# Optimization experiments

Measured on AMD Instinct MI355X. Metric: run time of the kernel, lower is better.

## Reference

```python
import jax, jax.numpy as jnp
import numpy as np

N_NODES = 100000
N_EDGES = 1600000
IN_CH = 64
HID = 64
OUT_CH = 128
EDGE_CH = 3
OBS_RANGE = 0.5
ATK_RANGE = 0.3


def setup_inputs() -> dict:
    key = jax.random.key(0)
    k = jax.random.split(key, 8)
    # node features: first column is an integer node type in {0,1,2}
    node_type = jax.random.randint(k[0], (N_NODES, 1), 0, 3).astype(jnp.float32)
    feats = jax.random.normal(k[1], (N_NODES, IN_CH - 1), dtype=jnp.float32)
    x = jnp.concatenate([node_type, feats], axis=-1)
    edge_index = jax.random.randint(k[2], (2, N_EDGES), 0, N_NODES)
    # edge_attr[:,0] = distance in [0,1)
    edge_attr = jax.random.uniform(k[3], (N_EDGES, EDGE_CH), dtype=jnp.float32)
    s1 = 1.0 / np.sqrt(2 * IN_CH + EDGE_CH)
    s2 = 1.0 / np.sqrt(HID)
    W1 = jax.random.normal(k[4], (2 * IN_CH + EDGE_CH, HID), dtype=jnp.float32) * s1
    b1 = jnp.zeros((HID,), dtype=jnp.float32)
    W2 = jax.random.normal(k[5], (HID, OUT_CH), dtype=jnp.float32) * s2
    b2 = jnp.zeros((OUT_CH,), dtype=jnp.float32)
    return {"x": x, "edge_index": edge_index, "edge_attr": edge_attr,
            "W1": W1, "b1": b1, "W2": W2, "b2": b2}


def reference(x, edge_index, edge_attr, W1, b1, W2, b2):
    src = edge_index[0]  # j (source)
    dst = edge_index[1]  # i (target)
    x_j = x[src]         # [E, IN_CH]
    x_i = x[dst]         # [E, IN_CH]
    h = jnp.concatenate([x_i, x_j, edge_attr], axis=-1)  # [E, 2*IN_CH+3]
    msg = jax.nn.relu(h @ W1 + b1) @ W2 + b2             # [E, OUT_CH]
    dist = edge_attr[:, 0]
    ntype = x_j[:, 0]
    mask = jnp.where(ntype == 0, dist < OBS_RANGE,
                     jnp.where(ntype == 1, dist < ATK_RANGE, True))
    msg = mask[:, None].astype(msg.dtype) * msg
    out = jax.ops.segment_sum(msg, dst, num_segments=x.shape[0])  # [N, OUT_CH]
    return jax.nn.relu(out)
```

## Files before the change

kernel.cpp:

```cpp
#include <hip/hip_runtime.h>

#define N_NODES 100000
#define N_EDGES 1600000
#define IN_CH   64
#define HID_CH  64
#define OUT_CH  128
#define TILE    128
#define N_TILES (N_EDGES / TILE)

typedef __attribute__((ext_vector_type(8))) __bf16    bf16x8;
typedef __attribute__((ext_vector_type(4))) float     f32x4;
typedef __attribute__((ext_vector_type(2))) _Float16  f16x2;
typedef __attribute__((ext_vector_type(8))) _Float16  f16x8;

__device__ __forceinline__ unsigned short f2bf(float f) {
    union { float f; unsigned int i; } c;
    c.f = f;
    unsigned int u = c.i;
    unsigned int r = (u + 0x7FFFu + ((u >> 16) & 1u)) >> 16;
    return (unsigned short)r;
}

__device__ __forceinline__ void atomic_pk_add_f16(unsigned int* addr, f16x2 val) {
    typedef __attribute__((address_space(1))) f16x2 gf16x2;
    __builtin_amdgcn_global_atomic_fadd_v2f16((gf16x2*)(void*)addr, val);
}

__global__ void gnn_prep(const float* __restrict__ xf,
                         unsigned short* __restrict__ xb,
                         uint4* __restrict__ hz,
                         float4* __restrict__ cz) {
    int i = blockIdx.x * blockDim.x + threadIdx.x;
    if (i < 1600000) {
        float4 v = reinterpret_cast<const float4*>(xf)[i];
        ushort4 o;
        o.x = f2bf(v.x); o.y = f2bf(v.y); o.z = f2bf(v.z); o.w = f2bf(v.w);
        reinterpret_cast<ushort4*>(xb)[i] = o;
    } else if (i < 2400000) {
        hz[i - 1600000] = (uint4){0u, 0u, 0u, 0u};
    } else if (i < 2425000) {
        cz[i - 2400000] = (float4){0.f, 0.f, 0.f, 0.f};
    }
}

__global__ __launch_bounds__(256, 4) void gnn_edge_hidden(
    const float*          __restrict__ x,
    const unsigned short* __restrict__ xb,
    const int*            __restrict__ eidx,
    const float*          __restrict__ ea,
    const float*          __restrict__ W1,
    const float*          __restrict__ b1,
    unsigned int*         __restrict__ hsum,
    float*                __restrict__ cnt)
{
    __shared__ __align__(16) unsigned short W1T[64][136];
    __shared__ float w1tail[4][64];
    __shared__ float eas[128][4];
    __shared__ float masks[128];
    __shared__ int   dsts[128];
    __shared__ int   srcs[128];

    const int tid  = threadIdx.x;
    const int wave = tid >> 6;
    const int lane = tid & 63;
    const int q    = lane >> 4;
    const int m16  = lane & 15;

    for (int idx = tid; idx < 128 * 64; idx += 256) {
        int k = idx >> 6, n = idx & 63;
        W1T[n][k] = f2bf(W1[idx]);
    }
    if (tid < 64) {
        w1tail[0][tid] = W1[128 * 64 + tid];
        w1tail[1][tid] = W1[129 * 64 + tid];
        w1tail[2][tid] = W1[130 * 64 + tid];
        w1tail[3][tid] = b1[tid];
    }

    for (int t = blockIdx.x; t < N_TILES; t += gridDim.x) {
        __syncthreads();
        if (tid < 128) {
            int e = t * TILE + tid;
            int s = eidx[e];
            int d = eidx[N_EDGES + e];
            srcs[tid] = s;
            dsts[tid] = d;
            float a0 = ea[e * 3 + 0];
            float a1 = ea[e * 3 + 1];
            float a2 = ea[e * 3 + 2];
            eas[tid][0] = a0; eas[tid][1] = a1; eas[tid][2] = a2;
            float nt = x[(size_t)s * IN_CH];
            float mk;
            if (nt == 0.0f)      mk = (a0 < 0.5f) ? 1.0f : 0.0f;
            else if (nt == 1.0f) mk = (a0 < 0.3f) ? 1.0f : 0.0f;
            else                 mk = 1.0f;
            masks[tid] = mk;
            if (mk != 0.0f) unsafeAtomicAdd(&cnt[d], 1.0f);
        }
        __syncthreads();

        const int ebase = wave * 32;

        f32x4 acc1[2][4];
#pragma unroll
        for (int mt = 0; mt < 2; ++mt) {
            float e0[4], e1[4], e2[4];
#pragma unroll
            for (int r = 0; r < 4; ++r) {
                int el = ebase + mt * 16 + q * 4 + r;
                e0[r] = eas[el][0]; e1[r] = eas[el][1]; e2[r] = eas[el][2];
            }
#pragma unroll
            for (int nt = 0; nt < 4; ++nt) {
                int n = nt * 16 + m16;
                float t0 = w1tail[0][n], t1 = w1tail[1][n];
                float t2 = w1tail[2][n], bb = w1tail[3][n];
#pragma unroll
                for (int r = 0; r < 4; ++r)
                    acc1[mt][nt][r] = bb + e0[r] * t0 + e1[r] * t1 + e2[r] * t2;
            }
        }

#pragma unroll
        for (int kc = 0; kc < 4; ++kc) {
            bf16x8 af[2];
#pragma unroll
            for (int mt = 0; mt < 2; ++mt) {
                int el   = ebase + mt * 16 + m16;
                int node = (kc < 2) ? dsts[el] : srcs[el];
                af[mt] = *reinterpret_cast<const bf16x8*>(
                    xb + (size_t)node * IN_CH + (kc & 1) * 32 + q * 8);
            }
#pragma unroll
            for (int nt = 0; nt < 4; ++nt) {
                bf16x8 bfr = *reinterpret_cast<const bf16x8*>(
                    &W1T[nt * 16 + m16][kc * 32 + q * 8]);
                acc1[0][nt] = __builtin_amdgcn_mfma_f32_16x16x32_bf16(af[0], bfr, acc1[0][nt], 0, 0, 0);
                acc1[1][nt] = __builtin_amdgcn_mfma_f32_16x16x32_bf16(af[1], bfr, acc1[1][nt], 0, 0, 0);
            }
        }

#pragma unroll
        for (int mt = 0; mt < 2; ++mt) {
#pragma unroll
            for (int r = 0; r < 4; ++r) {
                int el = ebase + mt * 16 + q * 4 + r;
                float mk = masks[el];
                if (mk != 0.0f) {
                    unsigned int* hbase = hsum + (size_t)dsts[el] * 32;
                    float v0 = acc1[mt][0][r]; v0 = v0 > 0.f ? v0 : 0.f;
                    float v1 = acc1[mt][1][r]; v1 = v1 > 0.f ? v1 : 0.f;
                    float v2 = acc1[mt][2][r]; v2 = v2 > 0.f ? v2 : 0.f;
                    float v3 = acc1[mt][3][r]; v3 = v3 > 0.f ? v3 : 0.f;
                    if (v0 + v1 > 0.f) {
                        f16x2 p01 = {(_Float16)v0, (_Float16)v1};
                        atomic_pk_add_f16(hbase + m16, p01);
                    }
                    if (v2 + v3 > 0.f) {
                        f16x2 p23 = {(_Float16)v2, (_Float16)v3};
                        atomic_pk_add_f16(hbase + 16 + m16, p23);
                    }
                }
            }
        }
    }
}

__global__ __launch_bounds__(256, 4) void gnn_node_out(
    const _Float16* __restrict__ hsum,
    const float*    __restrict__ cnt,
    const float*    __restrict__ W2,
    const float*    __restrict__ b2,
    float*          __restrict__ out)
{
    __shared__ __align__(16) unsigned short W2T[128][72];
    __shared__ float b2s[128];

    const int tid  = threadIdx.x;
    const int wave = tid >> 6;
    const int lane = tid & 63;
    const int q    = lane >> 4;
    const int m16  = lane & 15;

    for (int idx = tid; idx < 64 * 128; idx += 256) {
        int p = idx >> 7, n = idx & 127;
        int ch = (p >> 1) + 16 * (p & 1) + ((p >= 32) ? 16 : 0);
        W2T[n][p] = f2bf(W2[ch * 128 + n]);
    }
    if (tid < 128) b2s[tid] = b2[tid];
    __syncthreads();

    const int nodeBase = (blockIdx.x * 4 + wave) * 32;
    if (nodeBase >= N_NODES) return;

    f32x4 acc[2][8];
#pragma unroll
    for (int mt = 0; mt < 2; ++mt)
#pragma unroll
        for (int nt = 0; nt < 8; ++nt)
            acc[mt][nt] = (f32x4){0.0f, 0.0f, 0.0f, 0.0f};

#pragma unroll
    for (int kc = 0; kc < 2; ++kc) {
        bf16x8 af[2];
#pragma unroll
        for (int mt = 0; mt < 2; ++mt) {
            int node = nodeBase + mt * 16 + m16;
            if (node >= N_NODES) node = N_NODES - 1;
            f16x8 h = *reinterpret_cast<const f16x8*>(
                hsum + (size_t)node * HID_CH + kc * 32 + q * 8);
            union { bf16x8 v; unsigned short u[8]; } rr;
#pragma unroll
            for (int j = 0; j < 8; ++j) rr.u[j] = f2bf((float)h[j]);
            af[mt] = rr.v;
        }
#pragma unroll
        for (int nt = 0; nt < 8; ++nt) {
            bf16x8 bfr = *reinterpret_cast<const bf16x8*>(
                &W2T[nt * 16 + m16][kc * 32 + q * 8]);
            acc[0][nt] = __builtin_amdgcn_mfma_f32_16x16x32_bf16(af[0], bfr, acc[0][nt], 0, 0, 0);
            acc[1][nt] = __builtin_amdgcn_mfma_f32_16x16x32_bf16(af[1], bfr, acc[1][nt], 0, 0, 0);
        }
    }

#pragma unroll
    for (int mt = 0; mt < 2; ++mt) {
        float cc[4]; int nn[4];
#pragma unroll
        for (int r = 0; r < 4; ++r) {
            nn[r] = nodeBase + mt * 16 + q * 4 + r;
            cc[r] = (nn[r] < N_NODES) ? cnt[nn[r]] : 0.0f;
        }
#pragma unroll
        for (int nt = 0; nt < 8; ++nt) {
            int col = nt * 16 + m16;
            float bb = b2s[col];
#pragma unroll
            for (int r = 0; r < 4; ++r) {
                if (nn[r] < N_NODES) {
                    float v = acc[mt][nt][r] + cc[r] * bb;
                    out[(size_t)nn[r] * OUT_CH + col] = v > 0.0f ? v : 0.0f;
                }
            }
        }
    }
}

extern "C" void kernel_launch(void* const* d_in, const int* in_sizes, int n_in,
                              void* d_out, int out_size, void* d_ws, size_t ws_size,
                              hipStream_t stream) {
    const float* x  = (const float*)d_in[0];
    const int*   ei = (const int*)d_in[1];
    const float* ea = (const float*)d_in[2];
    const float* W1 = (const float*)d_in[3];
    const float* b1 = (const float*)d_in[4];
    const float* W2 = (const float*)d_in[5];
    const float* b2 = (const float*)d_in[6];
    float* out = (float*)d_out;

    char* wsb = (char*)d_ws;
    unsigned int*   hsum = (unsigned int*)wsb;
    float*          cnt  = (float*)(wsb + 12800000);
    unsigned short* xb   = (unsigned short*)(wsb + 13200000);

    gnn_prep<<<(2425000 + 255) / 256, 256, 0, stream>>>(
        x, xb, (uint4*)hsum, (float4*)cnt);

    gnn_edge_hidden<<<1024, 256, 0, stream>>>(x, xb, ei, ea, W1, b1, hsum, cnt);

    gnn_node_out<<<(N_NODES + 127) / 128, 256, 0, stream>>>(
        (const _Float16*)hsum, cnt, W2, b2, out);
}
```

Baseline: 281.4 us.

## Sort edges by destination and accumulate hidden sums in shared memory

Builds a CSR-like ordering of unmasked edges via histogram, three-pass scan and atomic scatter, packing source, destination and 10-bit quantized edge attributes into 8-byte records. The edge kernel then processes each block's contiguous destination range and accumulates ReLU hidden values with LDS float atomics before one f16 write per node. This removes the global packed-f16 atomics and zeroing of the hidden buffer, but adds several extra kernel launches, extra global passes over the edges, and quantization error on edge attributes.

```diff
diff --git a/kernel.cpp b/kernel.cpp
--- a/kernel.cpp
+++ b/kernel.cpp
@@ -5,8 +5,7 @@
 #define IN_CH   64
 #define HID_CH  64
 #define OUT_CH  128
-#define TILE    128
-#define N_TILES (N_EDGES / TILE)
+#define NPB     100
 
 typedef __attribute__((ext_vector_type(8))) __bf16    bf16x8;
 typedef __attribute__((ext_vector_type(4))) float     f32x4;
@@ -21,44 +20,113 @@
     return (unsigned short)r;
 }
 
-__device__ __forceinline__ void atomic_pk_add_f16(unsigned int* addr, f16x2 val) {
-    typedef __attribute__((address_space(1))) f16x2 gf16x2;
-    __builtin_amdgcn_global_atomic_fadd_v2f16((gf16x2*)(void*)addr, val);
-}
-
 __global__ void gnn_prep(const float* __restrict__ xf,
                          unsigned short* __restrict__ xb,
-                         uint4* __restrict__ hz,
-                         float4* __restrict__ cz) {
+                         unsigned char* __restrict__ ntype,
+                         uint4* __restrict__ degz) {
     int i = blockIdx.x * blockDim.x + threadIdx.x;
     if (i < 1600000) {
         float4 v = reinterpret_cast<const float4*>(xf)[i];
         ushort4 o;
         o.x = f2bf(v.x); o.y = f2bf(v.y); o.z = f2bf(v.z); o.w = f2bf(v.w);
         reinterpret_cast<ushort4*>(xb)[i] = o;
-    } else if (i < 2400000) {
-        hz[i - 1600000] = (uint4){0u, 0u, 0u, 0u};
-    } else if (i < 2425000) {
-        cz[i - 2400000] = (float4){0.f, 0.f, 0.f, 0.f};
-    }
-}
-
-__global__ __launch_bounds__(256, 4) void gnn_edge_hidden(
-    const float*          __restrict__ x,
+        if ((i & 15) == 0)
+            ntype[i >> 4] = (v.x == 0.0f) ? 0 : ((v.x == 1.0f) ? 1 : 2);
+    } else if (i < 1625000) {
+        degz[i - 1600000] = (uint4){0u, 0u, 0u, 0u};
+    }
+}
+
+__device__ __forceinline__ bool edge_mask(int ntc, float a0) {
+    if (ntc == 0) return a0 < 0.5f;
+    if (ntc == 1) return a0 < 0.3f;
+    return true;
+}
+
+__global__ void gnn_hist(const int* __restrict__ eidx,
+                         const float* __restrict__ ea,
+                         const unsigned char* __restrict__ ntype,
+                         int* __restrict__ deg) {
+    int e = blockIdx.x * blockDim.x + threadIdx.x;
+    if (e >= N_EDGES) return;
+    int s = eidx[e];
+    int d = eidx[N_EDGES + e];
+    if (edge_mask(ntype[s], ea[e * 3])) atomicAdd(&deg[d], 1);
+}
+
+__global__ void gnn_scanA(const int* __restrict__ deg,
+                          int* __restrict__ tmp, int* __restrict__ bsum) {
+    __shared__ int s[256];
+    int i = blockIdx.x * 256 + threadIdx.x;
+    int v = (i < N_NODES) ? deg[i] : 0;
+    s[threadIdx.x] = v;
+    for (int o = 1; o < 256; o <<= 1) {
+        __syncthreads();
+        int u = (threadIdx.x >= o) ? s[threadIdx.x - o] : 0;
+        __syncthreads();
+        s[threadIdx.x] += u;
+    }
+    __syncthreads();
+    if (i < N_NODES) tmp[i] = s[threadIdx.x];
+    if (threadIdx.x == 255) bsum[blockIdx.x] = s[255];
+}
+__global__ void gnn_scanB(const int* __restrict__ bsum, int* __restrict__ boff,
+                          int nblk) {
+    __shared__ int s[512];
+    int t = threadIdx.x;
+    int v = (t < nblk) ? bsum[t] : 0;
+    s[t] = v;
+    for (int o = 1; o < 512; o <<= 1) {
+        __syncthreads();
+        int u = (t >= o) ? s[t - o] : 0;
+        __syncthreads();
+        s[t] += u;
+    }
+    __syncthreads();
+    if (t < nblk) boff[t] = s[t] - v;
+}
+__global__ void gnn_scanC(const int* __restrict__ tmp, const int* __restrict__ deg,
+                          const int* __restrict__ boff, int* __restrict__ off) {
+    int i = blockIdx.x * 256 + threadIdx.x;
+    if (i < N_NODES) off[i] = tmp[i] - deg[i] + boff[blockIdx.x];
+}
+
+__global__ void gnn_scatter(const int* __restrict__ eidx,
+                            const float* __restrict__ ea,
+                            const unsigned char* __restrict__ ntype,
+                            int* __restrict__ off,
+                            uint2* __restrict__ rec) {
+    int e = blockIdx.x * blockDim.x + threadIdx.x;
+    if (e >= N_EDGES) return;
+    int s = eidx[e];
+    int d = eidx[N_EDGES + e];
+    float a0 = ea[e * 3], a1 = ea[e * 3 + 1], a2 = ea[e * 3 + 2];
+    if (!edge_mask(ntype[s], a0)) return;
+    int pos = atomicAdd(&off[d], 1);
+    unsigned a0q = (unsigned)(a0 * 1023.0f + 0.5f);
+    unsigned a1q = (unsigned)(a1 * 1023.0f + 0.5f);
+    unsigned a2q = (unsigned)(a2 * 1023.0f + 0.5f);
+    uint2 r;
+    r.x = (unsigned)s | (a0q << 17) | ((a1q & 31u) << 27);
+    r.y = (unsigned)d | ((a1q >> 5) << 17) | (a2q << 22);
+    rec[pos] = r;
+}
+
+__global__ __launch_bounds__(256) void gnn_edge_sorted(
     const unsigned short* __restrict__ xb,
-    const int*            __restrict__ eidx,
-    const float*          __restrict__ ea,
+    const uint2*          __restrict__ rec,
+    const int*            __restrict__ off,
     const float*          __restrict__ W1,
     const float*          __restrict__ b1,
-    unsigned int*         __restrict__ hsum,
-    float*                __restrict__ cnt)
+    unsigned int*         __restrict__ hsumU)
 {
     __shared__ __align__(16) unsigned short W1T[64][136];
     __shared__ float w1tail[4][64];
+    __shared__ float hloc[NPB * 68];
     __shared__ float eas[128][4];
-    __shared__ float masks[128];
-    __shared__ int   dsts[128];
     __shared__ int   srcs[128];
+    __shared__ int   dabs[128];
+    __shared__ int   dlocA[128];
 
     const int tid  = threadIdx.x;
     const int wave = tid >> 6;
@@ -76,26 +144,31 @@
         w1tail[2][tid] = W1[130 * 64 + tid];
         w1tail[3][tid] = b1[tid];
     }
-
-    for (int t = blockIdx.x; t < N_TILES; t += gridDim.x) {
-        __syncthreads();
+    for (int idx = tid; idx < NPB * 68; idx += 256) hloc[idx] = 0.0f;
+
+    const int nodeBase = blockIdx.x * NPB;
+    const int eStart = (nodeBase == 0) ? 0 : off[nodeBase - 1];
+    const int eEnd   = off[nodeBase + NPB - 1];
+    __syncthreads();
+
+    for (int te = eStart; te < eEnd; te += 128) {
         if (tid < 128) {
-            int e = t * TILE + tid;
-            int s = eidx[e];
-            int d = eidx[N_EDGES + e];
-            srcs[tid] = s;
-            dsts[tid] = d;
-            float a0 = ea[e * 3 + 0];
-            float a1 = ea[e * 3 + 1];
-            float a2 = ea[e * 3 + 2];
-            eas[tid][0] = a0; eas[tid][1] = a1; eas[tid][2] = a2;
-            float nt = x[(size_t)s * IN_CH];
-            float mk;
-            if (nt == 0.0f)      mk = (a0 < 0.5f) ? 1.0f : 0.0f;
-            else if (nt == 1.0f) mk = (a0 < 0.3f) ? 1.0f : 0.0f;
-            else                 mk = 1.0f;
-            masks[tid] = mk;
-            if (mk != 0.0f) unsafeAtomicAdd(&cnt[d], 1.0f);
+            int e = te + tid;
+            if (e < eEnd) {
+                uint2 r = rec[e];
+                int s = (int)(r.x & 0x1FFFFu);
+                int d = (int)(r.y & 0x1FFFFu);
+                srcs[tid]  = s;
+                dabs[tid]  = d;
+                dlocA[tid] = d - nodeBase;
+                const float dq = 1.0f / 1023.0f;
+                eas[tid][0] = (float)((r.x >> 17) & 1023u) * dq;
+                eas[tid][1] = (float)(((r.x >> 27) & 31u) | (((r.y >> 17) & 31u) << 5)) * dq;
+                eas[tid][2] = (float)((r.y >> 22) & 1023u) * dq;
+            } else {
+                srcs[tid] = 0; dabs[tid] = 0; dlocA[tid] = -1;
+                eas[tid][0] = 0.f; eas[tid][1] = 0.f; eas[tid][2] = 0.f;
+            }
         }
         __syncthreads();
 
@@ -127,7 +200,7 @@
 #pragma unroll
             for (int mt = 0; mt < 2; ++mt) {
                 int el   = ebase + mt * 16 + m16;
-                int node = (kc < 2) ? dsts[el] : srcs[el];
+                int node = (kc < 2) ? dabs[el] : srcs[el];
                 af[mt] = *reinterpret_cast<const bf16x8*>(
                     xb + (size_t)node * IN_CH + (kc & 1) * 32 + q * 8);
             }
@@ -145,30 +218,33 @@
 #pragma unroll
             for (int r = 0; r < 4; ++r) {
                 int el = ebase + mt * 16 + q * 4 + r;
-                float mk = masks[el];
-                if (mk != 0.0f) {
-                    unsigned int* hbase = hsum + (size_t)dsts[el] * 32;
-                    float v0 = acc1[mt][0][r]; v0 = v0 > 0.f ? v0 : 0.f;
-                    float v1 = acc1[mt][1][r]; v1 = v1 > 0.f ? v1 : 0.f;
-                    float v2 = acc1[mt][2][r]; v2 = v2 > 0.f ? v2 : 0.f;
-                    float v3 = acc1[mt][3][r]; v3 = v3 > 0.f ? v3 : 0.f;
-                    if (v0 + v1 > 0.f) {
-                        f16x2 p01 = {(_Float16)v0, (_Float16)v1};
-                        atomic_pk_add_f16(hbase + m16, p01);
-                    }
-                    if (v2 + v3 > 0.f) {
-                        f16x2 p23 = {(_Float16)v2, (_Float16)v3};
-                        atomic_pk_add_f16(hbase + 16 + m16, p23);
+                int dl = dlocA[el];
+                if (dl >= 0) {
+                    float* hr = &hloc[dl * 68 + m16];
+#pragma unroll
+                    for (int nt = 0; nt < 4; ++nt) {
+                        float v = acc1[mt][nt][r];
+                        if (v > 0.0f) atomicAdd(&hr[nt * 16], v);
                     }
                 }
             }
         }
+        __syncthreads();
+    }
+
+    __syncthreads();
+    for (int idx = tid; idx < NPB * 32; idx += 256) {
+        int ln = idx >> 5, c2 = idx & 31;
+        f16x2 p = {(_Float16)hloc[ln * 68 + c2 * 2],
+                   (_Float16)hloc[ln * 68 + c2 * 2 + 1]};
+        union { f16x2 v; unsigned u; } cv; cv.v = p;
+        hsumU[(size_t)(nodeBase + ln) * 32 + c2] = cv.u;
     }
 }
 
 __global__ __launch_bounds__(256, 4) void gnn_node_out(
     const _Float16* __restrict__ hsum,
-    const float*    __restrict__ cnt,
+    const int*      __restrict__ deg,
     const float*    __restrict__ W2,
     const float*    __restrict__ b2,
     float*          __restrict__ out)
@@ -183,9 +259,8 @@
     const int m16  = lane & 15;
 
     for (int idx = tid; idx < 64 * 128; idx += 256) {
-        int p = idx >> 7, n = idx & 127;
-        int ch = (p >> 1) + 16 * (p & 1) + ((p >= 32) ? 16 : 0);
-        W2T[n][p] = f2bf(W2[ch * 128 + n]);
+        int k = idx >> 7, n = idx & 127;
+        W2T[n][k] = f2bf(W2[k * 128 + n]);
     }
     if (tid < 128) b2s[tid] = b2[tid];
     __syncthreads();
@@ -229,7 +304,7 @@
 #pragma unroll
         for (int r = 0; r < 4; ++r) {
             nn[r] = nodeBase + mt * 16 + q * 4 + r;
-            cc[r] = (nn[r] < N_NODES) ? cnt[nn[r]] : 0.0f;
+            cc[r] = (nn[r] < N_NODES) ? (float)deg[nn[r]] : 0.0f;
         }
 #pragma unroll
         for (int nt = 0; nt < 8; ++nt) {
@@ -259,15 +334,26 @@
     float* out = (float*)d_out;
 
     char* wsb = (char*)d_ws;
-    unsigned int*   hsum = (unsigned int*)wsb;
-    float*          cnt  = (float*)(wsb + 12800000);
-    unsigned short* xb   = (unsigned short*)(wsb + 13200000);
-
-    gnn_prep<<<(2425000 + 255) / 256, 256, 0, stream>>>(
-        x, xb, (uint4*)hsum, (float4*)cnt);
-
-    gnn_edge_hidden<<<1024, 256, 0, stream>>>(x, xb, ei, ea, W1, b1, hsum, cnt);
-
+    unsigned short* xb    = (unsigned short*)(wsb);
+    unsigned char*  ntype = (unsigned char*)(wsb + 12800000);
+    int*            deg   = (int*)(wsb + 12902400);
+    int*            off   = (int*)(wsb + 13302400);
+    int*            tmp   = (int*)(wsb + 13702400);
+    int*            bsum  = (int*)(wsb + 14102400);
+    int*            boff  = (int*)(wsb + 14104448);
+    unsigned int*   hsumU = (unsigned int*)(wsb + 14106496);
+    uint2*          rec   = (uint2*)(wsb + 26906496);
+
+    const int nScanBlk = (N_NODES + 255) / 256;
+
+    gnn_prep<<<(1625000 + 255) / 256, 256, 0, stream>>>(
+        x, xb, ntype, (uint4*)deg);
+    gnn_hist<<<(N_EDGES + 255) / 256, 256, 0, stream>>>(ei, ea, ntype, deg);
+    gnn_scanA<<<nScanBlk, 256, 0, stream>>>(deg, tmp, bsum);
+    gnn_scanB<<<1, 512, 0, stream>>>(bsum, boff, nScanBlk);
+    gnn_scanC<<<nScanBlk, 256, 0, stream>>>(tmp, deg, boff, off);
+    gnn_scatter<<<(N_EDGES + 255) / 256, 256, 0, stream>>>(ei, ea, ntype, off, rec);
+    gnn_edge_sorted<<<N_NODES / NPB, 256, 0, stream>>>(xb, rec, off, W1, b1, hsumU);
     gnn_node_out<<<(N_NODES + 127) / 128, 256, 0, stream>>>(
-        (const _Float16*)hsum, cnt, W2, b2, out);
-}
+        (const _Float16*)hsumU, deg, W2, b2, out);
+}
```

After: 406.9 us. +44.6%, slower.
